# Performance work log

Hardware: AMD Instinct MI355X
Metric: run time of the kernel (lower is better)

Reference implementation:

```python
import jax, jax.numpy as jnp
import numpy as np

D = 512          # input_dim == hidden size of MinLSTM layers
OUT = 1          # output_dim of fc_out
B, T = 8, 4096
LN_EPS = 1e-5


def _linear_params(key, d_in, d_out):
    kw, kb = jax.random.split(key)
    lim = 1.0 / np.sqrt(d_in)
    W = jax.random.uniform(kw, (d_out, d_in), minval=-lim, maxval=lim, dtype=jnp.float32)
    b = jax.random.uniform(kb, (d_out,), minval=-lim, maxval=lim, dtype=jnp.float32)
    return W, b


def setup_inputs() -> dict:
    key = jax.random.key(0)
    ks = jax.random.split(key, 8)
    x = jax.random.normal(ks[0], (B, T, D), dtype=jnp.float32)
    Wf0, bf0 = _linear_params(ks[1], D, D)
    Wi0, bi0 = _linear_params(ks[2], D, D)
    Wh0, bh0 = _linear_params(ks[3], D, D)
    Wf1, bf1 = _linear_params(ks[4], D, D)
    Wi1, bi1 = _linear_params(ks[5], D, D)
    Wh1, bh1 = _linear_params(ks[6], D, D)
    W_out, b_out = _linear_params(ks[7], D, OUT)
    ln_g = jnp.ones((D,), dtype=jnp.float32)
    ln_b = jnp.zeros((D,), dtype=jnp.float32)
    return {
        'x': x,
        'Wf0': Wf0, 'bf0': bf0, 'Wi0': Wi0, 'bi0': bi0, 'Wh0': Wh0, 'bh0': bh0,
        'Wf1': Wf1, 'bf1': bf1, 'Wi1': Wi1, 'bi1': bi1, 'Wh1': Wh1, 'bh1': bh1,
        'ln_g': ln_g, 'ln_b': ln_b, 'W_out': W_out, 'b_out': b_out,
    }


def _minlstm(x, Wf, bf, Wi, bi, Wh, bh):
    # minLSTM (parallel form, h0 = 0):
    #   f = sigma(W_f x), i = sigma(W_i x), h~ = W_h x
    #   f' = f/(f+i), i' = i/(f+i)
    #   h_t = f'_t * h_{t-1} + i'_t * h~_t   (linear recurrence -> associative scan)
    f = jax.nn.sigmoid(jnp.einsum('btd,ed->bte', x, Wf) + bf)
    i = jax.nn.sigmoid(jnp.einsum('btd,ed->bte', x, Wi) + bi)
    h_tilde = jnp.einsum('btd,ed->bte', x, Wh) + bh
    denom = f + i
    a = f / denom                      # decay coefficient f'
    u = (i / denom) * h_tilde          # input contribution i' * h~

    def combine(c1, c2):
        a1, u1 = c1
        a2, u2 = c2
        return a1 * a2, a2 * u1 + u2

    _, h = jax.lax.associative_scan(combine, (a, u), axis=1)
    return h  # [B, T, D]


def reference(x, Wf0, bf0, Wi0, bi0, Wh0, bh0,
              Wf1, bf1, Wi1, bi1, Wh1, bh1,
              ln_g, ln_b, W_out, b_out):
    h = _minlstm(x, Wf0, bf0, Wi0, bi0, Wh0, bh0)
    h = _minlstm(h, Wf1, bf1, Wi1, bi1, Wh1, bh1)
    h = jnp.where(jnp.isnan(h), x, h)      # NaN fallback to input
    h = x + h                               # residual
    # LayerNorm over last dim
    mu = jnp.mean(h, axis=-1, keepdims=True)
    var = jnp.mean(jnp.square(h - mu), axis=-1, keepdims=True)
    hn = (h - mu) * jax.lax.rsqrt(var + LN_EPS) * ln_g + ln_b
    # output projection [B, T, OUT]
    return jnp.einsum('btd,od->bto', hn, W_out) + b_out
```

## Files before the change

### kernel.cpp

```cpp
#include <hip/hip_runtime.h>
#include <hip/hip_bf16.h>
#include <stdint.h>


#define MROWS 32768
#define DDIM  512
#define TLEN  4096
#define BSZ   8
#define NCHUNK 64
#define CLEN   64

typedef __attribute__((ext_vector_type(8))) __bf16 bf16x8;
typedef __attribute__((ext_vector_type(16))) float f32x16;
typedef __attribute__((ext_vector_type(4))) unsigned short ushort4_t;
typedef __attribute__((ext_vector_type(2))) unsigned short ushort2_t;

static __device__ __forceinline__ unsigned short f2bf(float f) {
    unsigned int u = __float_as_uint(f);
    u = (u + 0x7FFFu + ((u >> 16) & 1u)) >> 16;
    return (unsigned short)u;
}
static __device__ __forceinline__ void gload_lds16(const void* gptr, void* ldsp) {
    __builtin_amdgcn_global_load_lds(
        (const __attribute__((address_space(1))) uint32_t*)gptr,
        (__attribute__((address_space(3))) uint32_t*)ldsp,
        16, 0, 0);
}

#define WAITV(n) asm volatile("s_waitcnt vmcnt(" #n ")" ::: "memory")

__global__ __launch_bounds__(256) void cast_perm(
    const float* __restrict__ x,
    const float* __restrict__ w0, const float* __restrict__ w1,
    const float* __restrict__ w2, const float* __restrict__ w3,
    const float* __restrict__ w4, const float* __restrict__ w5,
    uint4* __restrict__ xp, uint4* __restrict__ wp)
{
    __shared__ unsigned short t[32 * 520];
    const int blk = blockIdx.x;
    const int tid = threadIdx.x;
    const float* src;
    uint4* dst;
    if (blk < 1024) {
        src = x + (size_t)blk * 32 * 512;
        dst = xp + (size_t)blk * 2048;
    } else {
        int gb = blk - 1024;
        int g = gb >> 4;
        const float* w = (g == 0) ? w0 : (g == 1) ? w1 : (g == 2) ? w2
                       : (g == 3) ? w3 : (g == 4) ? w4 : w5;
        src = w + (size_t)(gb & 15) * 32 * 512;
        dst = wp + (size_t)gb * 2048;
    }
#pragma unroll
    for (int p = 0; p < 16; ++p) {
        int idx = p * 256 + tid;
        int r = idx >> 7, c4 = idx & 127;
        float4 v = reinterpret_cast<const float4*>(src)[(size_t)r * 128 + c4];
        ushort4_t o;
        o.x = f2bf(v.x); o.y = f2bf(v.y); o.z = f2bf(v.z); o.w = f2bf(v.w);
        *reinterpret_cast<ushort4_t*>(&t[r * 520 + c4 * 4]) = o;
    }
    __syncthreads();
#pragma unroll
    for (int q = 0; q < 8; ++q) {
        int s = q * 256 + tid;
        int Tk = s >> 8, c = (s >> 5) & 7, r = s & 31;
        uint4 o = *reinterpret_cast<const uint4*>(&t[r * 520 + Tk * 64 + c * 8]);
        dst[s] = o;
    }
}

__global__ __launch_bounds__(256, 2) void gates_gemm(
    const unsigned short* __restrict__ X,
    const unsigned short* __restrict__ Wf,
    const unsigned short* __restrict__ Wi,
    const unsigned short* __restrict__ Wh,
    const float* __restrict__ bf_, const float* __restrict__ bi_,
    const float* __restrict__ bh_,
    unsigned int* __restrict__ au_out,
    float* __restrict__ Asum, float* __restrict__ Usum)
{
    __shared__ __align__(16) unsigned short lds[2 * 20480];

    const int tid  = threadIdx.x;
    const int lane = tid & 63;
    const int wave = tid >> 6;
    const int wm = wave >> 1;
    const int wn = wave & 1;
    const int ln31 = lane & 31;
    const int kh = lane >> 5;

    const int w = blockIdx.x;
    const int xcd = w & 7;
    const int s = w >> 3;
    const int by = xcd * 32 + (s >> 3);
    const int bx = s & 7;
    const int mblk = by * 128;
    const int nblk = bx * 64;

    const int grA = mblk >> 5;
    const int gnB = nblk >> 5;
    const unsigned short* gA0 = X  + ((size_t)(grA + 0) * 2048 + tid) * 8;
    const unsigned short* gA1 = X  + ((size_t)(grA + 1) * 2048 + tid) * 8;
    const unsigned short* gA2 = X  + ((size_t)(grA + 2) * 2048 + tid) * 8;
    const unsigned short* gA3 = X  + ((size_t)(grA + 3) * 2048 + tid) * 8;
    const unsigned short* gF0 = Wf + ((size_t)(gnB + 0) * 2048 + tid) * 8;
    const unsigned short* gF1 = Wf + ((size_t)(gnB + 1) * 2048 + tid) * 8;
    const unsigned short* gI0 = Wi + ((size_t)(gnB + 0) * 2048 + tid) * 8;
    const unsigned short* gI1 = Wi + ((size_t)(gnB + 1) * 2048 + tid) * 8;
    const unsigned short* gH0 = Wh + ((size_t)(gnB + 0) * 2048 + tid) * 8;
    const unsigned short* gH1 = Wh + ((size_t)(gnB + 1) * 2048 + tid) * 8;

    const int tid8 = tid * 8;
    const int lane16 = lane * 8;

    f32x16 accF[2], accI[2], accH[2];
#pragma unroll
    for (int mi = 0; mi < 2; ++mi) {
#pragma unroll
        for (int e = 0; e < 16; ++e) { accF[mi][e] = 0.f; accI[mi][e] = 0.f; accH[mi][e] = 0.f; }
    }

#define STAGE(bb) do { \
    gload_lds16(gA0, lds + (bb) + tid8);             \
    gload_lds16(gA1, lds + (bb) + 2048  + tid8);     \
    gload_lds16(gA2, lds + (bb) + 4096  + tid8);     \
    gload_lds16(gA3, lds + (bb) + 6144  + tid8);     \
    gload_lds16(gF0, lds + (bb) + 8192  + tid8);     \
    gload_lds16(gF1, lds + (bb) + 10240 + tid8);     \
    gload_lds16(gI0, lds + (bb) + 12288 + tid8);     \
    gload_lds16(gI1, lds + (bb) + 14336 + tid8);     \
    gload_lds16(gH0, lds + (bb) + 16384 + tid8);     \
    gload_lds16(gH1, lds + (bb) + 18432 + tid8);     \
    gA0 += 2048; gA1 += 2048; gA2 += 2048; gA3 += 2048; gF0 += 2048; \
    gF1 += 2048; gI0 += 2048; gI1 += 2048; gH0 += 2048; gH1 += 2048; } while (0)

    STAGE(0);

#pragma unroll
    for (int t = 0; t < 8; ++t) {
        if (t < 7) {
            STAGE(((t + 1) & 1) * 20480);
            WAITV(10);
        } else {
            WAITV(0);
        }
        __builtin_amdgcn_s_barrier();
        __builtin_amdgcn_sched_barrier(0);

        const unsigned short* cb = lds + (t & 1) * 20480;
#pragma unroll
        for (int ks = 0; ks < 4; ++ks) {
            bf16x8 af0 = *reinterpret_cast<const bf16x8*>(cb + (wm * 8 + ks) * 512 + lane16);
            bf16x8 bF  = *reinterpret_cast<const bf16x8*>(cb + 8192  + (wn * 4 + ks) * 512 + lane16);
            bf16x8 af1 = *reinterpret_cast<const bf16x8*>(cb + (wm * 8 + 4 + ks) * 512 + lane16);
            bf16x8 bI  = *reinterpret_cast<const bf16x8*>(cb + 12288 + (wn * 4 + ks) * 512 + lane16);
            bf16x8 bH  = *reinterpret_cast<const bf16x8*>(cb + 16384 + (wn * 4 + ks) * 512 + lane16);
            __builtin_amdgcn_s_setprio(1);
            accF[0] = __builtin_amdgcn_mfma_f32_32x32x16_bf16(af0, bF, accF[0], 0, 0, 0);
            accF[1] = __builtin_amdgcn_mfma_f32_32x32x16_bf16(af1, bF, accF[1], 0, 0, 0);
            accI[0] = __builtin_amdgcn_mfma_f32_32x32x16_bf16(af0, bI, accI[0], 0, 0, 0);
            accI[1] = __builtin_amdgcn_mfma_f32_32x32x16_bf16(af1, bI, accI[1], 0, 0, 0);
            accH[0] = __builtin_amdgcn_mfma_f32_32x32x16_bf16(af0, bH, accH[0], 0, 0, 0);
            accH[1] = __builtin_amdgcn_mfma_f32_32x32x16_bf16(af1, bH, accH[1], 0, 0, 0);
            __builtin_amdgcn_s_setprio(0);
        }
        __builtin_amdgcn_sched_barrier(0);
        __builtin_amdgcn_s_barrier();
        __builtin_amdgcn_sched_barrier(0);
    }
#undef STAGE

    const int n = nblk + wn * 32 + ln31;
    const float bfv = bf_[n], biv = bi_[n], bhv = bh_[n];
    const bool up = (lane & 32) != 0;
    float ca = 1.f, cu = 0.f;
#pragma unroll
    for (int mi = 0; mi < 2; ++mi) {
#pragma unroll
        for (int j = 0; j < 4; ++j) {
            float sa = 1.f, su = 0.f;
#pragma unroll
            for (int r = 0; r < 4; ++r) {
                const int reg = 4 * j + r;
                const int m = mblk + wm * 64 + mi * 32 + 8 * j + 4 * kh + r;
                float zf = accF[mi][reg] + bfv;
                float zi = accI[mi][reg] + biv;
                float zh = accH[mi][reg] + bhv;
                float ef = __expf(-zf);
                float ei = __expf(-zi);
                float inv = __frcp_rn(2.0f + ef + ei);
                float av = (1.0f + ei) * inv;
                float uv = (1.0f + ef) * inv * zh;
                au_out[(size_t)m * 512 + n] =
                    ((unsigned int)f2bf(uv) << 16) | (unsigned int)f2bf(av);
                su = av * su + uv; sa *= av;
            }
            float oa = __shfl_xor(sa, 32), ou = __shfl_xor(su, 32);
            float ta = sa * oa;
            float tu = up ? (sa * ou + su) : (oa * su + ou);
            cu = ta * cu + tu; ca = ca * ta;
        }
    }
    if (lane < 32) {
        size_t ci = (size_t)(by * 2 + wm) * 512 + n;
        Asum[ci] = ca;
        Usum[ci] = cu;
    }
}

__global__ __launch_bounds__(256) void scan_pass2(
    const float4* __restrict__ Asum, const float4* __restrict__ Usum,
    float4* __restrict__ Hinit)
{
    int gid = blockIdx.x * 256 + threadIdx.x;
    int col = gid >> 3;
    int t8  = gid & 7;
    int b = col >> 7, d4 = col & 127;
    int lane = threadIdx.x & 63;

    float4 a[8], u[8];
    float4 Ac = {1.f, 1.f, 1.f, 1.f}, Uc = {0.f, 0.f, 0.f, 0.f};
#pragma unroll
    for (int j = 0; j < 8; ++j) {
        size_t idx = (size_t)(b * 64 + t8 * 8 + j) * 128 + d4;
        a[j] = Asum[idx]; u[j] = Usum[idx];
        Uc.x = a[j].x * Uc.x + u[j].x; Uc.y = a[j].y * Uc.y + u[j].y;
        Uc.z = a[j].z * Uc.z + u[j].z; Uc.w = a[j].w * Uc.w + u[j].w;
        Ac.x *= a[j].x; Ac.y *= a[j].y; Ac.z *= a[j].z; Ac.w *= a[j].w;
    }
#pragma unroll
    for (int d = 1; d < 8; d <<= 1) {
        float4 Ao, Uo;
        Ao.x = __shfl(Ac.x, lane - d); Ao.y = __shfl(Ac.y, lane - d);
        Ao.z = __shfl(Ac.z, lane - d); Ao.w = __shfl(Ac.w, lane - d);
        Uo.x = __shfl(Uc.x, lane - d); Uo.y = __shfl(Uc.y, lane - d);
        Uo.z = __shfl(Uc.z, lane - d); Uo.w = __shfl(Uc.w, lane - d);
        if (t8 >= d) {
            Uc.x = Ac.x * Uo.x + Uc.x; Uc.y = Ac.y * Uo.y + Uc.y;
            Uc.z = Ac.z * Uo.z + Uc.z; Uc.w = Ac.w * Uo.w + Uc.w;
            Ac.x *= Ao.x; Ac.y *= Ao.y; Ac.z *= Ao.z; Ac.w *= Ao.w;
        }
    }
    float4 h;
    h.x = __shfl(Uc.x, lane - 1); h.y = __shfl(Uc.y, lane - 1);
    h.z = __shfl(Uc.z, lane - 1); h.w = __shfl(Uc.w, lane - 1);
    if (t8 == 0) { h.x = 0.f; h.y = 0.f; h.z = 0.f; h.w = 0.f; }
#pragma unroll
    for (int j = 0; j < 8; ++j) {
        size_t idx = (size_t)(b * 64 + t8 * 8 + j) * 128 + d4;
        Hinit[idx] = h;
        h.x = a[j].x * h.x + u[j].x; h.y = a[j].y * h.y + u[j].y;
        h.z = a[j].z * h.z + u[j].z; h.w = a[j].w * h.w + u[j].w;
    }
}

__global__ void scan_pass3(const uint4* __restrict__ au,
                           const float4* __restrict__ Hinit,
                           uint4* __restrict__ hp) {
    int gid = blockIdx.x * 256 + threadIdx.x;
    int d8 = gid & 63;
    int c  = (gid >> 6) & 63;
    int b  = gid >> 12;
    const int base_m = b * TLEN + c * CLEN;
    size_t aubase = (size_t)base_m * 128 + d8 * 2;
    size_t s4 = (size_t)(b * NCHUNK + c) * 128 + d8 * 2;
    float4 h0 = Hinit[s4], h1 = Hinit[s4 + 1];
    float h[8] = {h0.x, h0.y, h0.z, h0.w, h1.x, h1.y, h1.z, h1.w};
    const int Tk = d8 >> 3, cc = d8 & 7;
    for (int l = 0; l < CLEN; ++l) {
        int m = base_m + l;
        uint4 a0 = au[aubase + (size_t)l * 128];
        uint4 a1 = au[aubase + (size_t)l * 128 + 1];
        unsigned vv[8] = {a0.x, a0.y, a0.z, a0.w, a1.x, a1.y, a1.z, a1.w};
        unsigned ob[8];
#pragma unroll
        for (int j = 0; j < 8; ++j) {
            float av = __uint_as_float(vv[j] << 16);
            float uv = __uint_as_float(vv[j] & 0xFFFF0000u);
            h[j] = av * h[j] + uv;
            ob[j] = f2bf(h[j]);
        }
        uint4 o;
        o.x = ob[0] | (ob[1] << 16);
        o.y = ob[2] | (ob[3] << 16);
        o.z = ob[4] | (ob[5] << 16);
        o.w = ob[6] | (ob[7] << 16);
        int S = (m >> 5) * 2048 + Tk * 256 + cc * 32 + (m & 31);
        hp[S] = o;
    }
}

__global__ __launch_bounds__(256) void scan3_final(
    const uint2* __restrict__ au2, const float2* __restrict__ Hinit2,
    const float2* __restrict__ x2,
    const float* __restrict__ g, const float* __restrict__ bvec,
    const float* __restrict__ Wout, const float* __restrict__ bout,
    float* __restrict__ out)
{
    __shared__ unsigned short rl[64 * 512];
    const int blk = blockIdx.x;
    const int b = blk >> 6, c = blk & 63;
    const int d2 = threadIdx.x;

    float2 h0 = Hinit2[(size_t)blk * 256 + d2];
    float h[2] = {h0.x, h0.y};
    size_t base = ((size_t)b * TLEN + c * CLEN) * 256 + d2;

#pragma unroll 4
    for (int l = 0; l < CLEN; ++l) {
        size_t idx = base + (size_t)l * 256;
        uint2 v = au2[idx];
        float2 xr = x2[idx];
        const unsigned vv[2] = {v.x, v.y};
        const float xa[2] = {xr.x, xr.y};
        ushort2_t o;
#pragma unroll
        for (int j = 0; j < 2; ++j) {
            float av = __uint_as_float(vv[j] << 16);
            float uv = __uint_as_float(vv[j] & 0xFFFF0000u);
            h[j] = av * h[j] + uv;
            float hv = h[j];
            if (hv != hv) hv = xa[j];
            o[j] = f2bf(xa[j] + hv);
        }
        *reinterpret_cast<ushort2_t*>(&rl[l * 512 + d2 * 2]) = o;
    }
    __syncthreads();

    const int lane = threadIdx.x & 63;
    const int wv = threadIdx.x >> 6;
    float4 g0 = reinterpret_cast<const float4*>(g)[lane * 2];
    float4 g1 = reinterpret_cast<const float4*>(g)[lane * 2 + 1];
    float4 b0 = reinterpret_cast<const float4*>(bvec)[lane * 2];
    float4 b1 = reinterpret_cast<const float4*>(bvec)[lane * 2 + 1];
    float4 w0 = reinterpret_cast<const float4*>(Wout)[lane * 2];
    float4 w1 = reinterpret_cast<const float4*>(Wout)[lane * 2 + 1];
    const float gg[8] = {g0.x, g0.y, g0.z, g0.w, g1.x, g1.y, g1.z, g1.w};
    const float bb[8] = {b0.x, b0.y, b0.z, b0.w, b1.x, b1.y, b1.z, b1.w};
    const float ww[8] = {w0.x, w0.y, w0.z, w0.w, w1.x, w1.y, w1.z, w1.w};
    const float bo = bout[0];

    for (int rr = 0; rr < 16; ++rr) {
        const int row = wv * 16 + rr;
        uint4 rv = *reinterpret_cast<const uint4*>(&rl[row * 512 + lane * 8]);
        const unsigned rw[4] = {rv.x, rv.y, rv.z, rv.w};
        float r[8];
#pragma unroll
        for (int j = 0; j < 4; ++j) {
            r[2 * j]     = __uint_as_float(rw[j] << 16);
            r[2 * j + 1] = __uint_as_float(rw[j] & 0xFFFF0000u);
        }
        float s = 0.f, q = 0.f;
#pragma unroll
        for (int j = 0; j < 8; ++j) { s += r[j]; q += r[j] * r[j]; }
#pragma unroll
        for (int m = 32; m >= 1; m >>= 1) {
            s += __shfl_xor(s, m);
            q += __shfl_xor(q, m);
        }
        float mu = s * (1.0f / 512.0f);
        float var = q * (1.0f / 512.0f) - mu * mu;
        float rstd = rsqrtf(var + 1e-5f);
        float p = 0.f;
#pragma unroll
        for (int j = 0; j < 8; ++j)
            p += ((r[j] - mu) * rstd * gg[j] + bb[j]) * ww[j];
#pragma unroll
        for (int m = 32; m >= 1; m >>= 1) p += __shfl_xor(p, m);
        if (lane == 0)
            out[(size_t)b * TLEN + c * CLEN + row] = p + bo;
    }
}

extern "C" void kernel_launch(void* const* d_in, const int* in_sizes, int n_in,
                              void* d_out, int out_size, void* d_ws, size_t ws_size,
                              hipStream_t stream) {
    const float* x    = (const float*)d_in[0];
    const float* Wf0  = (const float*)d_in[1];  const float* bf0 = (const float*)d_in[2];
    const float* Wi0  = (const float*)d_in[3];  const float* bi0 = (const float*)d_in[4];
    const float* Wh0  = (const float*)d_in[5];  const float* bh0 = (const float*)d_in[6];
    const float* Wf1  = (const float*)d_in[7];  const float* bf1 = (const float*)d_in[8];
    const float* Wi1  = (const float*)d_in[9];  const float* bi1 = (const float*)d_in[10];
    const float* Wh1  = (const float*)d_in[11]; const float* bh1 = (const float*)d_in[12];
    const float* ln_g = (const float*)d_in[13]; const float* ln_b = (const float*)d_in[14];
    const float* W_out = (const float*)d_in[15]; const float* b_out = (const float*)d_in[16];

    char* ws = (char*)d_ws;
    unsigned short* Xp = (unsigned short*)ws;  ws += (size_t)MROWS * DDIM * 2;
    unsigned short* Wp = (unsigned short*)ws;  ws += (size_t)6 * DDIM * DDIM * 2;
    unsigned int* aubuf = (unsigned int*)ws;   ws += (size_t)MROWS * DDIM * 4;
    float* Asum = (float*)ws;  ws += (size_t)BSZ * NCHUNK * DDIM * 4;
    float* Usum = (float*)ws;  ws += (size_t)BSZ * NCHUNK * DDIM * 4;
    float* Hinit = (float*)ws; ws += (size_t)BSZ * NCHUNK * DDIM * 4;
    unsigned short* h0p = (unsigned short*)ws; ws += (size_t)MROWS * DDIM * 2;

    const size_t GSTRIDE = (size_t)DDIM * DDIM;

    cast_perm<<<1120, 256, 0, stream>>>(
        x, Wf0, Wi0, Wh0, Wf1, Wi1, Wh1, (uint4*)Xp, (uint4*)Wp);

    gates_gemm<<<2048, 256, 0, stream>>>(Xp, Wp, Wp + GSTRIDE, Wp + 2 * GSTRIDE,
                                         bf0, bi0, bh0, aubuf, Asum, Usum);
    scan_pass2<<<32, 256, 0, stream>>>((const float4*)Asum, (const float4*)Usum, (float4*)Hinit);
    scan_pass3<<<128, 256, 0, stream>>>((const uint4*)aubuf, (const float4*)Hinit, (uint4*)h0p);

    gates_gemm<<<2048, 256, 0, stream>>>(h0p, Wp + 3 * GSTRIDE, Wp + 4 * GSTRIDE, Wp + 5 * GSTRIDE,
                                         bf1, bi1, bh1, aubuf, Asum, Usum);
    scan_pass2<<<32, 256, 0, stream>>>((const float4*)Asum, (const float4*)Usum, (float4*)Hinit);
    scan3_final<<<512, 256, 0, stream>>>((const uint2*)aubuf, (const float2*)Hinit,
                                         (const float2*)x, ln_g, ln_b, W_out, b_out,
                                         (float*)d_out);
}
```

Measured before the change: 208.0 us.

## Interleave next-tile global-to-LDS loads across k-substeps of the MFMA loop

The gate GEMM loop used to issue all ten global-to-LDS loads for the next tile at the top of each iteration. They are now split into three groups, issued one per k-substep, with a barrier before every substep and an explicit LDS wait before each MFMA group. The aim is to spread memory traffic more evenly alongside the matrix instructions and to reduce bursty issue. In exchange it adds four barriers per tile instead of two, and the forced lgkmcnt(0) wait stops LDS reads for the next substep from overlapping with the current MFMAs.

```diff
diff --git a/kernel.cpp b/kernel.cpp
--- a/kernel.cpp
+++ b/kernel.cpp
@@ -28,6 +28,7 @@
 }
 
 #define WAITV(n) asm volatile("s_waitcnt vmcnt(" #n ")" ::: "memory")
+#define WAITL0() asm volatile("s_waitcnt lgkmcnt(0)" ::: "memory")
 
 __global__ __launch_bounds__(256) void cast_perm(
     const float* __restrict__ x,
@@ -122,41 +123,43 @@
         for (int e = 0; e < 16; ++e) { accF[mi][e] = 0.f; accI[mi][e] = 0.f; accH[mi][e] = 0.f; }
     }
 
-#define STAGE(bb) do { \
-    gload_lds16(gA0, lds + (bb) + tid8);             \
-    gload_lds16(gA1, lds + (bb) + 2048  + tid8);     \
-    gload_lds16(gA2, lds + (bb) + 4096  + tid8);     \
-    gload_lds16(gA3, lds + (bb) + 6144  + tid8);     \
-    gload_lds16(gF0, lds + (bb) + 8192  + tid8);     \
-    gload_lds16(gF1, lds + (bb) + 10240 + tid8);     \
-    gload_lds16(gI0, lds + (bb) + 12288 + tid8);     \
-    gload_lds16(gI1, lds + (bb) + 14336 + tid8);     \
-    gload_lds16(gH0, lds + (bb) + 16384 + tid8);     \
-    gload_lds16(gH1, lds + (bb) + 18432 + tid8);     \
-    gA0 += 2048; gA1 += 2048; gA2 += 2048; gA3 += 2048; gF0 += 2048; \
-    gF1 += 2048; gI0 += 2048; gI1 += 2048; gH0 += 2048; gH1 += 2048; } while (0)
-
-    STAGE(0);
+#define STAGE_C0(bb) do { \
+    gload_lds16(gA0, lds + (bb) + tid8);         gA0 += 2048; \
+    gload_lds16(gA1, lds + (bb) + 2048  + tid8); gA1 += 2048; \
+    gload_lds16(gA2, lds + (bb) + 4096  + tid8); gA2 += 2048; \
+    gload_lds16(gA3, lds + (bb) + 6144  + tid8); gA3 += 2048; } while (0)
+#define STAGE_C1(bb) do { \
+    gload_lds16(gF0, lds + (bb) + 8192  + tid8); gF0 += 2048; \
+    gload_lds16(gF1, lds + (bb) + 10240 + tid8); gF1 += 2048; \
+    gload_lds16(gI0, lds + (bb) + 12288 + tid8); gI0 += 2048; } while (0)
+#define STAGE_C2(bb) do { \
+    gload_lds16(gI1, lds + (bb) + 14336 + tid8); gI1 += 2048; \
+    gload_lds16(gH0, lds + (bb) + 16384 + tid8); gH0 += 2048; \
+    gload_lds16(gH1, lds + (bb) + 18432 + tid8); gH1 += 2048; } while (0)
+
+    STAGE_C0(0); STAGE_C1(0); STAGE_C2(0);
 
 #pragma unroll
     for (int t = 0; t < 8; ++t) {
-        if (t < 7) {
-            STAGE(((t + 1) & 1) * 20480);
-            WAITV(10);
-        } else {
-            WAITV(0);
-        }
-        __builtin_amdgcn_s_barrier();
-        __builtin_amdgcn_sched_barrier(0);
-
         const unsigned short* cb = lds + (t & 1) * 20480;
-#pragma unroll
-        for (int ks = 0; ks < 4; ++ks) {
-            bf16x8 af0 = *reinterpret_cast<const bf16x8*>(cb + (wm * 8 + ks) * 512 + lane16);
-            bf16x8 bF  = *reinterpret_cast<const bf16x8*>(cb + 8192  + (wn * 4 + ks) * 512 + lane16);
-            bf16x8 af1 = *reinterpret_cast<const bf16x8*>(cb + (wm * 8 + 4 + ks) * 512 + lane16);
-            bf16x8 bI  = *reinterpret_cast<const bf16x8*>(cb + 12288 + (wn * 4 + ks) * 512 + lane16);
-            bf16x8 bH  = *reinterpret_cast<const bf16x8*>(cb + 16384 + (wn * 4 + ks) * 512 + lane16);
+        const int nbb = ((t + 1) & 1) * 20480;
+#pragma unroll
+        for (int p = 0; p < 4; ++p) {
+            if (p == 0) { WAITV(0); }
+            __builtin_amdgcn_s_barrier();
+            __builtin_amdgcn_sched_barrier(0);
+            if (t < 7) {
+                if (p == 0) STAGE_C0(nbb);
+                else if (p == 1) STAGE_C1(nbb);
+                else if (p == 2) STAGE_C2(nbb);
+            }
+            bf16x8 af0 = *reinterpret_cast<const bf16x8*>(cb + (wm * 8 + p) * 512 + lane16);
+            bf16x8 bF  = *reinterpret_cast<const bf16x8*>(cb + 8192  + (wn * 4 + p) * 512 + lane16);
+            bf16x8 af1 = *reinterpret_cast<const bf16x8*>(cb + (wm * 8 + 4 + p) * 512 + lane16);
+            bf16x8 bI  = *reinterpret_cast<const bf16x8*>(cb + 12288 + (wn * 4 + p) * 512 + lane16);
+            bf16x8 bH  = *reinterpret_cast<const bf16x8*>(cb + 16384 + (wn * 4 + p) * 512 + lane16);
+            WAITL0();
+            __builtin_amdgcn_sched_barrier(0);
             __builtin_amdgcn_s_setprio(1);
             accF[0] = __builtin_amdgcn_mfma_f32_32x32x16_bf16(af0, bF, accF[0], 0, 0, 0);
             accF[1] = __builtin_amdgcn_mfma_f32_32x32x16_bf16(af1, bF, accF[1], 0, 0, 0);
@@ -165,12 +168,12 @@
             accH[0] = __builtin_amdgcn_mfma_f32_32x32x16_bf16(af0, bH, accH[0], 0, 0, 0);
             accH[1] = __builtin_amdgcn_mfma_f32_32x32x16_bf16(af1, bH, accH[1], 0, 0, 0);
             __builtin_amdgcn_s_setprio(0);
-        }
-        __builtin_amdgcn_sched_barrier(0);
-        __builtin_amdgcn_s_barrier();
-        __builtin_amdgcn_sched_barrier(0);
-    }
-#undef STAGE
+            __builtin_amdgcn_sched_barrier(0);
+        }
+    }
+#undef STAGE_C0
+#undef STAGE_C1
+#undef STAGE_C2
 
     const int n = nblk + wn * 32 + ln31;
     const float bfv = bf_[n], biv = bi_[n], bhv = bh_[n];
```

Result: no change. 207.8 us (-0.1%).
